# Performance work log

Hardware: AMD Instinct MI355X
Metric: run time of the kernel (lower is better)

## Reference

```python
import jax, jax.numpy as jnp
import numpy as np

NUM_HEAD = 4
BN_EPS = 1e-3


def conv2d(x, w, groups=1, padding=0):
    # x: NCHW, w: OIHW
    return jax.lax.conv_general_dilated(
        x, w, window_strides=(1, 1), padding=[(padding, padding)] * 2,
        dimension_numbers=('NCHW', 'OIHW', 'NCHW'), feature_group_count=groups)


def bn_eval(x, gamma, beta, mean, var):
    # BatchNorm2d in eval mode, eps=0.001
    s = gamma / jnp.sqrt(var + BN_EPS)
    return x * s[None, :, None, None] + (beta - mean * s)[None, :, None, None]


def setup_inputs() -> dict:
    key = jax.random.key(0)
    ks = jax.random.split(key, 8)
    ch = 256
    qkv_out = 2 * ch  # ch + dim_key*num_head*2 with dim_key = ch//num_head//2
    inp = {
        'x': jax.random.normal(ks[0], (8, ch, 48, 48), jnp.float32),
        'qkv_w': jax.random.normal(ks[1], (qkv_out, ch, 1, 1), jnp.float32) * 0.05,
        'qkv_g': jnp.ones((qkv_out,), jnp.float32),
        'qkv_b': jnp.zeros((qkv_out,), jnp.float32),
        'qkv_m': jax.random.normal(ks[2], (qkv_out,), jnp.float32) * 0.1,
        'qkv_v': jax.random.uniform(ks[3], (qkv_out,), jnp.float32) + 0.5,
        'c1_w': jax.random.normal(ks[4], (ch, 1, 3, 3), jnp.float32) * 0.1,
        'c1_g': jnp.ones((ch,), jnp.float32),
        'c1_b': jnp.zeros((ch,), jnp.float32),
        'c1_m': jnp.zeros((ch,), jnp.float32),
        'c1_v': jnp.ones((ch,), jnp.float32),
        'c2_w': jax.random.normal(ks[5], (ch, ch, 1, 1), jnp.float32) * 0.05,
        'c2_g': jnp.ones((ch,), jnp.float32),
        'c2_b': jnp.zeros((ch,), jnp.float32),
        'c2_m': jnp.zeros((ch,), jnp.float32),
        'c2_v': jnp.ones((ch,), jnp.float32),
    }
    return inp


def reference(x, qkv_w, qkv_g, qkv_b, qkv_m, qkv_v,
              c1_w, c1_g, c1_b, c1_m, c1_v,
              c2_w, c2_g, c2_b, c2_m, c2_v):
    b, c, h, w = x.shape
    hw = h * w
    dim_head = c // NUM_HEAD
    dim_key = dim_head // 2
    scale = dim_key ** (-0.5)

    qkv = bn_eval(conv2d(x, qkv_w), qkv_g, qkv_b, qkv_m, qkv_v)
    qkv = qkv.reshape(b, NUM_HEAD, 2 * dim_key + dim_head, hw)
    q = qkv[:, :, :dim_key]                 # (b, nh, dk, hw)
    k = qkv[:, :, dim_key:2 * dim_key]      # (b, nh, dk, hw)
    v = qkv[:, :, 2 * dim_key:]             # (b, nh, dh, hw)

    attn = jnp.einsum('bnki,bnkj->bnij', q, k) * scale  # (b, nh, hw, hw)
    attn = jax.nn.softmax(attn, axis=-1)
    out = jnp.einsum('bndj,bnij->bndi', v, attn).reshape(b, c, h, w)

    v_img = v.reshape(b, c, h, w)
    out = out + bn_eval(conv2d(v_img, c1_w, groups=c, padding=1), c1_g, c1_b, c1_m, c1_v)
    return bn_eval(conv2d(out, c2_w), c2_g, c2_b, c2_m, c2_v)
```

## Files before the change

kernel.cpp:

```cpp
#include <hip/hip_runtime.h>
#include <math.h>

#define HW 2304
#define NB 8
#define CH 256
#define QC 512
#define NH 4
#define DK 32
#define DV 64
#define EPS 1e-3f

typedef __bf16 bf16;
typedef bf16 bf16x8 __attribute__((ext_vector_type(8)));
typedef bf16 bf16x4 __attribute__((ext_vector_type(4)));
typedef float f32x4 __attribute__((ext_vector_type(4)));

#define QSC (0.17677669529663687f * 1.4426950408889634f)

__global__ __launch_bounds__(256) void wprep(
    const float* __restrict__ qkv_w, const float* __restrict__ qkv_g,
    const float* __restrict__ qkv_b, const float* __restrict__ qkv_m,
    const float* __restrict__ qkv_v,
    const float* __restrict__ c1_w, const float* __restrict__ c1_g,
    const float* __restrict__ c1_b, const float* __restrict__ c1_m,
    const float* __restrict__ c1_v,
    const float* __restrict__ c2_w, const float* __restrict__ c2_g,
    const float* __restrict__ c2_b, const float* __restrict__ c2_m,
    const float* __restrict__ c2_v,
    bf16* __restrict__ Wq, float* __restrict__ bq,
    bf16* __restrict__ W2, float* __restrict__ b2,
    float* __restrict__ W1)
{
  const int tid = blockIdx.x * 256 + threadIdx.x;
  {
    const int co = tid >> 8;
    const float s = qkv_g[co] / sqrtf(qkv_v[co] + EPS);
    const float f = ((co & 127) < DK) ? QSC : 1.f;
    Wq[tid] = (bf16)(qkv_w[tid] * s * f);
  }
  if (tid < 65536) {
    const int co = tid >> 8;
    const float s = c2_g[co] / sqrtf(c2_v[co] + EPS);
    W2[tid] = (bf16)(c2_w[tid] * s);
  }
  if (tid < 2560) {
    const int c = tid / 10, k = tid - c * 10;
    const float s = c1_g[c] / sqrtf(c1_v[c] + EPS);
    float v;
    if (k < 9) v = c1_w[c * 9 + k] * s;
    else       v = c1_b[c] - c1_m[c] * s;
    W1[tid] = v;
  }
  if (tid < QC) {
    const float s = qkv_g[tid] / sqrtf(qkv_v[tid] + EPS);
    const float f = ((tid & 127) < DK) ? QSC : 1.f;
    bq[tid] = (qkv_b[tid] - qkv_m[tid] * s) * f;
  }
  if (tid < CH) {
    const float s = c2_g[tid] / sqrtf(c2_v[tid] + EPS);
    b2[tid] = c2_b[tid] - c2_m[tid] * s;
  }
}

__global__ __launch_bounds__(256) void xprep(
    const float* __restrict__ x, bf16* __restrict__ Xt)
{
  __shared__ float T[64][65];
  const int t = threadIdx.x;
  const int p0 = blockIdx.x * 64;
  const int ci0 = blockIdx.y * 64;
  const int b = blockIdx.z;
  #pragma unroll
  for (int r = 0; r < 4; ++r) {
    const int e = t + 256 * r;
    const int ci = e >> 4, p4 = (e & 15) * 4;
    const float4 v = *reinterpret_cast<const float4*>(
        x + ((size_t)(b * CH + ci0 + ci)) * HW + p0 + p4);
    T[ci][p4 + 0] = v.x; T[ci][p4 + 1] = v.y;
    T[ci][p4 + 2] = v.z; T[ci][p4 + 3] = v.w;
  }
  __syncthreads();
  #pragma unroll
  for (int r = 0; r < 2; ++r) {
    const int e = t + 256 * r;
    const int p = e >> 3, c8 = (e & 7) * 8;
    bf16x8 pk;
    #pragma unroll
    for (int j = 0; j < 8; ++j) pk[j] = (bf16)T[c8 + j][p];
    *reinterpret_cast<bf16x8*>(Xt + ((size_t)b * HW + p0 + p) * CH + ci0 + c8) = pk;
  }
}

__global__ __launch_bounds__(256) void qkv_gemm(
    const bf16* __restrict__ Xt, const bf16* __restrict__ Wq,
    const float* __restrict__ bq,
    bf16* __restrict__ Qb, bf16* __restrict__ Kb, bf16* __restrict__ Vb)
{
  const int t = threadIdx.x;
  const int wv = t >> 6, l = t & 63, li = l & 15, g = l >> 4;
  const int cow = blockIdx.y * 64 + wv * 16;
  const int p0 = blockIdx.x * 64;
  const int b = blockIdx.z;
  const bf16* Bb = Xt + ((size_t)b * HW + p0) * CH;
  const bf16* Ab = Wq + (size_t)(cow + li) * CH + g * 8;
  f32x4 acc[4] = {{0.f,0.f,0.f,0.f},{0.f,0.f,0.f,0.f},
                  {0.f,0.f,0.f,0.f},{0.f,0.f,0.f,0.f}};
  #pragma unroll
  for (int k0 = 0; k0 < CH; k0 += 32) {
    const bf16x8 af = *reinterpret_cast<const bf16x8*>(Ab + k0);
    #pragma unroll
    for (int pt = 0; pt < 4; ++pt) {
      const bf16x8 bfr = *reinterpret_cast<const bf16x8*>(
          Bb + (size_t)(pt * 16 + li) * CH + k0 + g * 8);
      acc[pt] = __builtin_amdgcn_mfma_f32_16x16x32_bf16(af, bfr, acc[pt], 0, 0, 0);
    }
  }
  const float4 bv = *reinterpret_cast<const float4*>(bq + cow + g * 4);
  const int r0 = cow & 127;
  const int h = cow >> 7;
  const int bh = b * NH + h;
  if (r0 < 2 * DK) {
    bf16* dst = (r0 < DK) ? Qb : Kb;
    const int kk0 = (r0 & 31) + g * 4;
    #pragma unroll
    for (int pt = 0; pt < 4; ++pt) {
      bf16x4 pk;
      pk[0] = (bf16)(acc[pt][0] + bv.x); pk[1] = (bf16)(acc[pt][1] + bv.y);
      pk[2] = (bf16)(acc[pt][2] + bv.z); pk[3] = (bf16)(acc[pt][3] + bv.w);
      *reinterpret_cast<bf16x4*>(
          dst + ((size_t)bh * HW + p0 + pt * 16 + li) * DK + kk0) = pk;
    }
  } else {
    const int d0 = (r0 - 2 * DK) + g * 4;
    #pragma unroll
    for (int pt = 0; pt < 4; ++pt) {
      const int p = p0 + pt * 16 + li;
      Vb[((size_t)bh * DV + d0 + 0) * HW + p] = (bf16)(acc[pt][0] + bv.x);
      Vb[((size_t)bh * DV + d0 + 1) * HW + p] = (bf16)(acc[pt][1] + bv.y);
      Vb[((size_t)bh * DV + d0 + 2) * HW + p] = (bf16)(acc[pt][2] + bv.z);
      Vb[((size_t)bh * DV + d0 + 3) * HW + p] = (bf16)(acc[pt][3] + bv.w);
    }
  }
}

__global__ __launch_bounds__(256) void flash_attn(
    const bf16* __restrict__ Qb, const bf16* __restrict__ Kb,
    const bf16* __restrict__ Vb, const float* __restrict__ W1,
    bf16* __restrict__ F)
{
  __shared__ bf16 Plds[4][16][136];
  __shared__ float wdw[DV][10];
  const int t = threadIdx.x;
  const int wv = t >> 6;
  const int l = t & 63;
  const int li = l & 15;
  const int gq = l >> 4;
  const int bh = blockIdx.y;
  const int b = bh >> 2, h = bh & 3;
  const int i0 = blockIdx.x * 64 + wv * 16;

  for (int e = t; e < DV * 10; e += 256) {
    const int d = e / 10, k = e - d * 10;
    wdw[d][k] = W1[(h * DV + d) * 10 + k];
  }
  __syncthreads();

  const bf16x8 qf = *reinterpret_cast<const bf16x8*>(
      Qb + ((size_t)bh * HW + i0 + li) * DK + gq * 8);
  const bf16* Kbase = Kb + (size_t)bh * HW * DK;
  const bf16* Vbase = Vb + (size_t)bh * DV * HW;

  f32x4 acc[4] = {{0.f,0.f,0.f,0.f},{0.f,0.f,0.f,0.f},
                  {0.f,0.f,0.f,0.f},{0.f,0.f,0.f,0.f}};
  float m_run = -INFINITY, l_run = 0.f;

  for (int j0 = 0; j0 < HW; j0 += 128) {
    f32x4 st[8];
    #pragma unroll
    for (int jt = 0; jt < 8; ++jt) {
      const bf16x8 kf = *reinterpret_cast<const bf16x8*>(
          Kbase + (size_t)(j0 + jt * 16 + li) * DK + gq * 8);
      st[jt] = __builtin_amdgcn_mfma_f32_16x16x32_bf16(
          kf, qf, (f32x4){0.f,0.f,0.f,0.f}, 0, 0, 0);
    }
    float tm = -INFINITY;
    #pragma unroll
    for (int jt = 0; jt < 8; ++jt)
      #pragma unroll
      for (int r = 0; r < 4; ++r) tm = fmaxf(tm, st[jt][r]);
    tm = fmaxf(tm, __shfl_xor(tm, 16));
    tm = fmaxf(tm, __shfl_xor(tm, 32));
    const float mnew = fmaxf(m_run, tm);
    const float corr = __builtin_exp2f(m_run - mnew);
    m_run = mnew;
    l_run *= corr;
    #pragma unroll
    for (int dt = 0; dt < 4; ++dt)
      #pragma unroll
      for (int r = 0; r < 4; ++r) acc[dt][r] *= corr;
    float ps = 0.f;
    #pragma unroll
    for (int jt = 0; jt < 8; ++jt) {
      bf16x4 pb;
      #pragma unroll
      for (int r = 0; r < 4; ++r) {
        const float pv = __builtin_exp2f(st[jt][r] - mnew);
        ps += pv;
        pb[r] = (bf16)pv;
      }
      *reinterpret_cast<bf16x4*>(&Plds[wv][li][jt * 16 + gq * 4]) = pb;
    }
    ps += __shfl_xor(ps, 16);
    ps += __shfl_xor(ps, 32);
    l_run += ps;
    #pragma unroll
    for (int kt = 0; kt < 4; ++kt) {
      const bf16x8 pf = *reinterpret_cast<const bf16x8*>(
          &Plds[wv][li][kt * 32 + gq * 8]);
      #pragma unroll
      for (int dt = 0; dt < 4; ++dt) {
        const bf16x8 vf = *reinterpret_cast<const bf16x8*>(
            Vbase + (size_t)(dt * 16 + li) * HW + j0 + kt * 32 + gq * 8);
        acc[dt] = __builtin_amdgcn_mfma_f32_16x16x32_bf16(vf, pf, acc[dt], 0, 0, 0);
      }
    }
  }
  const float inv = 1.f / l_run;
  const int i = i0 + li;
  const int y = i / 48, xx = i - y * 48;
  bf16* Fo = F + ((size_t)b * HW + i) * CH + h * DV;
  #pragma unroll
  for (int dt = 0; dt < 4; ++dt) {
    bf16x4 pk;
    #pragma unroll
    for (int r = 0; r < 4; ++r) {
      const int d = dt * 16 + gq * 4 + r;
      const bf16* vrow = Vbase + (size_t)d * HW;
      float a = wdw[d][9];
      #pragma unroll
      for (int ky = 0; ky < 3; ++ky) {
        const int yy = y + ky - 1;
        const bool vy = (unsigned)yy < 48u;
        const int yc = vy ? yy : y;
        #pragma unroll
        for (int kx = 0; kx < 3; ++kx) {
          const int x2 = xx + kx - 1;
          const bool vx = (unsigned)x2 < 48u;
          const float wk = (vy && vx) ? wdw[d][ky * 3 + kx] : 0.f;
          const int nb = yc * 48 + (vx ? x2 : xx);
          a = fmaf(wk, (float)vrow[nb], a);
        }
      }
      pk[r] = (bf16)(acc[dt][r] * inv + a);
    }
    *reinterpret_cast<bf16x4*>(Fo + dt * 16 + gq * 4) = pk;
  }
}

__global__ __launch_bounds__(256) void c2_gemm(
    const bf16* __restrict__ F, const bf16* __restrict__ W2,
    const float* __restrict__ b2, float* __restrict__ out)
{
  const int t = threadIdx.x;
  const int wv = t >> 6, l = t & 63, li = l & 15, g = l >> 4;
  const int cow = blockIdx.y * 64 + wv * 16;
  const int p0 = blockIdx.x * 64;
  const int b = blockIdx.z;
  const bf16* Bb = F + ((size_t)b * HW + p0) * CH;
  const bf16* Ab = W2 + (size_t)(cow + li) * CH + g * 8;
  f32x4 acc[4] = {{0.f,0.f,0.f,0.f},{0.f,0.f,0.f,0.f},
                  {0.f,0.f,0.f,0.f},{0.f,0.f,0.f,0.f}};
  #pragma unroll
  for (int k0 = 0; k0 < CH; k0 += 32) {
    const bf16x8 af = *reinterpret_cast<const bf16x8*>(Ab + k0);
    #pragma unroll
    for (int pt = 0; pt < 4; ++pt) {
      const bf16x8 bfr = *reinterpret_cast<const bf16x8*>(
          Bb + (size_t)(pt * 16 + li) * CH + k0 + g * 8);
      acc[pt] = __builtin_amdgcn_mfma_f32_16x16x32_bf16(af, bfr, acc[pt], 0, 0, 0);
    }
  }
  const float4 bv = *reinterpret_cast<const float4*>(b2 + cow + g * 4);
  #pragma unroll
  for (int pt = 0; pt < 4; ++pt) {
    const int p = p0 + pt * 16 + li;
    float* ob = out + ((size_t)b * CH + cow + g * 4) * HW + p;
    ob[0 * HW] = acc[pt][0] + bv.x;
    ob[1 * HW] = acc[pt][1] + bv.y;
    ob[2 * HW] = acc[pt][2] + bv.z;
    ob[3 * HW] = acc[pt][3] + bv.w;
  }
}

extern "C" void kernel_launch(void* const* d_in, const int* in_sizes, int n_in,
                              void* d_out, int out_size, void* d_ws, size_t ws_size,
                              hipStream_t stream)
{
  const float* x     = (const float*)d_in[0];
  const float* qkv_w = (const float*)d_in[1];
  const float* qkv_g = (const float*)d_in[2];
  const float* qkv_b = (const float*)d_in[3];
  const float* qkv_m = (const float*)d_in[4];
  const float* qkv_v = (const float*)d_in[5];
  const float* c1_w  = (const float*)d_in[6];
  const float* c1_g  = (const float*)d_in[7];
  const float* c1_b  = (const float*)d_in[8];
  const float* c1_m  = (const float*)d_in[9];
  const float* c1_v  = (const float*)d_in[10];
  const float* c2_w  = (const float*)d_in[11];
  const float* c2_g  = (const float*)d_in[12];
  const float* c2_b  = (const float*)d_in[13];
  const float* c2_m  = (const float*)d_in[14];
  const float* c2_v  = (const float*)d_in[15];
  float* out = (float*)d_out;

  char* wp = (char*)d_ws;
  bf16* Qb = (bf16*)wp;  wp += (size_t)NB * NH * HW * DK * 2;
  bf16* Kb = (bf16*)wp;  wp += (size_t)NB * NH * HW * DK * 2;
  bf16* Vb = (bf16*)wp;  wp += (size_t)NB * NH * DV * HW * 2;
  bf16* Xt = (bf16*)wp;  wp += (size_t)NB * HW * CH * 2;
  bf16* F  = (bf16*)wp;  wp += (size_t)NB * HW * CH * 2;
  bf16* Wq = (bf16*)wp;  wp += (size_t)QC * CH * 2;
  bf16* W2 = (bf16*)wp;  wp += (size_t)CH * CH * 2;
  float* bq = (float*)wp; wp += QC * 4;
  float* b2 = (float*)wp; wp += CH * 4;
  float* W1 = (float*)wp; wp += CH * 10 * 4;

  wprep<<<dim3(512), 256, 0, stream>>>(qkv_w, qkv_g, qkv_b, qkv_m, qkv_v,
                                       c1_w, c1_g, c1_b, c1_m, c1_v,
                                       c2_w, c2_g, c2_b, c2_m, c2_v,
                                       Wq, bq, W2, b2, W1);
  xprep<<<dim3(36, 4, 8), 256, 0, stream>>>(x, Xt);
  qkv_gemm<<<dim3(36, 8, 8), 256, 0, stream>>>(Xt, Wq, bq, Qb, Kb, Vb);
  flash_attn<<<dim3(36, 32), 256, 0, stream>>>(Qb, Kb, Vb, W1, F);
  c2_gemm<<<dim3(36, 4, 8), 256, 0, stream>>>(F, W2, b2, out);
}
```

Baseline: 461.1 us.

## Split attention KV range across two wave groups and hoist depthwise conv into own kernel

Flash attention blocks now use 512 threads: two groups of four waves each process half of the key range, then merge their partial softmax states (max, sum, accumulators) through LDS. K fragments are prefetched one tile ahead in registers. The 3x3 depthwise conv moves out of the attention epilogue into a separate vectorized kernel that writes a bf16 buffer, which attention reads back. The intent is more waves in flight to hide latency and an epilogue free of scattered gathers. The cost is an extra launch, extra memory traffic for the new buffer, and more register pressure.

Measured after the change: 388.9 us. 15.7% less time.

```diff
diff --git a/kernel.cpp b/kernel.cpp
--- a/kernel.cpp
+++ b/kernel.cpp
@@ -143,27 +143,62 @@
   }
 }
 
-__global__ __launch_bounds__(256) void flash_attn(
+__global__ __launch_bounds__(256) void dwc(
+    const bf16* __restrict__ Vb, const float* __restrict__ W1,
+    bf16* __restrict__ Dw)
+{
+  const int gid = blockIdx.x * 256 + threadIdx.x;
+  const int c = gid / 288;
+  const int ck = gid - c * 288;
+  const int p0 = ck * 8;
+  const int y = p0 / 48, x0 = p0 - y * 48;
+  const float* wc = W1 + (c & 255) * 10;
+  float w[9];
+  #pragma unroll
+  for (int k = 0; k < 9; ++k) w[k] = wc[k];
+  float o[8];
+  #pragma unroll
+  for (int j = 0; j < 8; ++j) o[j] = wc[9];
+  const bf16* vch = Vb + (size_t)c * HW;
+  #pragma unroll
+  for (int ky = 0; ky < 3; ++ky) {
+    const int yy = y + ky - 1;
+    if (yy < 0 || yy >= 48) continue;
+    const bf16* row = vch + yy * 48 + x0;
+    const bf16x8 mid = *reinterpret_cast<const bf16x8*>(row);
+    float v[10];
+    v[0] = (x0 > 0)  ? (float)row[-1] : 0.f;
+    #pragma unroll
+    for (int j = 0; j < 8; ++j) v[j + 1] = (float)mid[j];
+    v[9] = (x0 < 40) ? (float)row[8]  : 0.f;
+    #pragma unroll
+    for (int kx = 0; kx < 3; ++kx) {
+      const float wk = w[ky * 3 + kx];
+      #pragma unroll
+      for (int j = 0; j < 8; ++j) o[j] = fmaf(wk, v[j + kx], o[j]);
+    }
+  }
+  bf16x8 pk;
+  #pragma unroll
+  for (int j = 0; j < 8; ++j) pk[j] = (bf16)o[j];
+  *reinterpret_cast<bf16x8*>(Dw + (size_t)c * HW + p0) = pk;
+}
+
+__global__ __launch_bounds__(512) void flash_attn(
     const bf16* __restrict__ Qb, const bf16* __restrict__ Kb,
-    const bf16* __restrict__ Vb, const float* __restrict__ W1,
+    const bf16* __restrict__ Vb, const bf16* __restrict__ Dw,
     bf16* __restrict__ F)
 {
-  __shared__ bf16 Plds[4][16][136];
-  __shared__ float wdw[DV][10];
+  __shared__ bf16 Plds[8][16][136];
   const int t = threadIdx.x;
   const int wv = t >> 6;
   const int l = t & 63;
   const int li = l & 15;
   const int gq = l >> 4;
+  const int it = wv & 3, jh = wv >> 2;
   const int bh = blockIdx.y;
   const int b = bh >> 2, h = bh & 3;
-  const int i0 = blockIdx.x * 64 + wv * 16;
-
-  for (int e = t; e < DV * 10; e += 256) {
-    const int d = e / 10, k = e - d * 10;
-    wdw[d][k] = W1[(h * DV + d) * 10 + k];
-  }
-  __syncthreads();
+  const int i0 = blockIdx.x * 64 + it * 16;
 
   const bf16x8 qf = *reinterpret_cast<const bf16x8*>(
       Qb + ((size_t)bh * HW + i0 + li) * DK + gq * 8);
@@ -174,15 +209,27 @@
                   {0.f,0.f,0.f,0.f},{0.f,0.f,0.f,0.f}};
   float m_run = -INFINITY, l_run = 0.f;
 
-  for (int j0 = 0; j0 < HW; j0 += 128) {
+  const int jbeg = jh * (HW / 2);
+  const int jend = jbeg + (HW / 2);
+
+  bf16x8 kc[8];
+  #pragma unroll
+  for (int jt = 0; jt < 8; ++jt)
+    kc[jt] = *reinterpret_cast<const bf16x8*>(
+        Kbase + (size_t)(jbeg + jt * 16 + li) * DK + gq * 8);
+
+  for (int j0 = jbeg; j0 < jend; j0 += 128) {
     f32x4 st[8];
     #pragma unroll
-    for (int jt = 0; jt < 8; ++jt) {
-      const bf16x8 kf = *reinterpret_cast<const bf16x8*>(
-          Kbase + (size_t)(j0 + jt * 16 + li) * DK + gq * 8);
+    for (int jt = 0; jt < 8; ++jt)
       st[jt] = __builtin_amdgcn_mfma_f32_16x16x32_bf16(
-          kf, qf, (f32x4){0.f,0.f,0.f,0.f}, 0, 0, 0);
-    }
+          kc[jt], qf, (f32x4){0.f,0.f,0.f,0.f}, 0, 0, 0);
+    const int jn = (j0 + 128 < jend) ? (j0 + 128) : jbeg;
+    #pragma unroll
+    for (int jt = 0; jt < 8; ++jt)
+      kc[jt] = *reinterpret_cast<const bf16x8*>(
+          Kbase + (size_t)(jn + jt * 16 + li) * DK + gq * 8);
+
     float tm = -INFINITY;
     #pragma unroll
     for (int jt = 0; jt < 8; ++jt)
@@ -225,35 +272,44 @@
       }
     }
   }
-  const float inv = 1.f / l_run;
-  const int i = i0 + li;
-  const int y = i / 48, xx = i - y * 48;
-  bf16* Fo = F + ((size_t)b * HW + i) * CH + h * DV;
-  #pragma unroll
-  for (int dt = 0; dt < 4; ++dt) {
-    bf16x4 pk;
-    #pragma unroll
-    for (int r = 0; r < 4; ++r) {
-      const int d = dt * 16 + gq * 4 + r;
-      const bf16* vrow = Vbase + (size_t)d * HW;
-      float a = wdw[d][9];
-      #pragma unroll
-      for (int ky = 0; ky < 3; ++ky) {
-        const int yy = y + ky - 1;
-        const bool vy = (unsigned)yy < 48u;
-        const int yc = vy ? yy : y;
-        #pragma unroll
-        for (int kx = 0; kx < 3; ++kx) {
-          const int x2 = xx + kx - 1;
-          const bool vx = (unsigned)x2 < 48u;
-          const float wk = (vy && vx) ? wdw[d][ky * 3 + kx] : 0.f;
-          const int nb = yc * 48 + (vx ? x2 : xx);
-          a = fmaf(wk, (float)vrow[nb], a);
-        }
+
+  __syncthreads();
+  float* cacc = (float*)&Plds[0][0][0];
+  float* cml  = cacc + 4 * 64 * 17;
+  if (jh == 1) {
+    float* dst = cacc + (wv - 4) * 64 * 17 + l * 17;
+    #pragma unroll
+    for (int dt = 0; dt < 4; ++dt)
+      #pragma unroll
+      for (int r = 0; r < 4; ++r) dst[dt * 4 + r] = acc[dt][r];
+    if (gq == 0) {
+      cml[(wv - 4) * 32 + li] = m_run;
+      cml[(wv - 4) * 32 + 16 + li] = l_run;
+    }
+  }
+  __syncthreads();
+  if (jh == 0) {
+    const float* src = cacc + wv * 64 * 17 + l * 17;
+    const float mb = cml[wv * 32 + li];
+    const float lb = cml[wv * 32 + 16 + li];
+    const float m = fmaxf(m_run, mb);
+    const float ca = __builtin_exp2f(m_run - m);
+    const float cb = __builtin_exp2f(mb - m);
+    const float linv = 1.f / (l_run * ca + lb * cb);
+    const int i = i0 + li;
+    const bf16* dwb = Dw + (size_t)bh * DV * HW + i;
+    bf16* Fo = F + ((size_t)b * HW + i) * CH + h * DV;
+    #pragma unroll
+    for (int dt = 0; dt < 4; ++dt) {
+      bf16x4 pk;
+      #pragma unroll
+      for (int r = 0; r < 4; ++r) {
+        const int d = dt * 16 + gq * 4 + r;
+        const float oa = (acc[dt][r] * ca + src[dt * 4 + r] * cb) * linv;
+        pk[r] = (bf16)(oa + (float)dwb[(size_t)d * HW]);
       }
-      pk[r] = (bf16)(acc[dt][r] * inv + a);
-    }
-    *reinterpret_cast<bf16x4*>(Fo + dt * 16 + gq * 4) = pk;
+      *reinterpret_cast<bf16x4*>(Fo + dt * 16 + gq * 4) = pk;
+    }
   }
 }
 
@@ -320,6 +376,7 @@
   bf16* Vb = (bf16*)wp;  wp += (size_t)NB * NH * DV * HW * 2;
   bf16* Xt = (bf16*)wp;  wp += (size_t)NB * HW * CH * 2;
   bf16* F  = (bf16*)wp;  wp += (size_t)NB * HW * CH * 2;
+  bf16* Dw = (bf16*)wp;  wp += (size_t)NB * NH * DV * HW * 2;
   bf16* Wq = (bf16*)wp;  wp += (size_t)QC * CH * 2;
   bf16* W2 = (bf16*)wp;  wp += (size_t)CH * CH * 2;
   float* bq = (float*)wp; wp += QC * 4;
@@ -332,6 +389,7 @@
                                        Wq, bq, W2, b2, W1);
   xprep<<<dim3(36, 4, 8), 256, 0, stream>>>(x, Xt);
   qkv_gemm<<<dim3(36, 8, 8), 256, 0, stream>>>(Xt, Wq, bq, Qb, Kb, Vb);
-  flash_attn<<<dim3(36, 32), 256, 0, stream>>>(Qb, Kb, Vb, W1, F);
+  dwc<<<dim3(2304), 256, 0, stream>>>(Vb, W1, Dw);
+  flash_attn<<<dim3(36, 32), 512, 0, stream>>>(Qb, Kb, Vb, Dw, F);
   c2_gemm<<<dim3(36, 4, 8), 256, 0, stream>>>(F, W2, b2, out);
 }
```
